# Kernel tuning notes

Hardware: AMD Instinct MI355X
Metric: run time of the kernel (lower is better)

Reference implementation:

```python
import jax, jax.numpy as jnp
import numpy as np

H = 128
EPS = 1e-5
INFERENCE_BIAS = 0.1


def setup_inputs() -> dict:
    key = jax.random.key(0)
    ks = jax.random.split(key, 10)
    n_users, n_foods, E = 100000, 50000, 1000000
    z_user = jax.random.normal(ks[0], (n_users, H), dtype=jnp.float32)
    z_food = jax.random.normal(ks[1], (n_foods, H), dtype=jnp.float32)
    row = jax.random.randint(ks[2], (E,), 0, n_users, dtype=jnp.int64)
    col = jax.random.randint(ks[3], (E,), 0, n_foods, dtype=jnp.int64)
    # lin1: Linear(2H -> H); lin2: Linear(H -> 1)
    W1 = jax.random.normal(ks[4], (H, 2 * H), dtype=jnp.float32) * (1.0 / np.sqrt(2 * H))
    b1 = jnp.zeros((H,), dtype=jnp.float32)
    gamma = jnp.ones((H,), dtype=jnp.float32)
    beta = jnp.zeros((H,), dtype=jnp.float32)
    running_mean = jax.random.normal(ks[5], (H,), dtype=jnp.float32) * 0.1
    running_var = jnp.abs(jax.random.normal(ks[6], (H,), dtype=jnp.float32)) * 0.1 + 1.0
    W2 = jax.random.normal(ks[7], (1, H), dtype=jnp.float32) * (1.0 / np.sqrt(H))
    b2 = jnp.zeros((1,), dtype=jnp.float32)
    return {"z_user": z_user, "z_food": z_food, "row": row, "col": col,
            "W1": W1, "b1": b1, "gamma": gamma, "beta": beta,
            "running_mean": running_mean, "running_var": running_var,
            "W2": W2, "b2": b2}


def reference(z_user, z_food, row, col, W1, b1, gamma, beta,
              running_mean, running_var, W2, b2):
    # gather per-edge endpoint embeddings and concat: [E, 2H]
    z = jnp.concatenate([z_user[row], z_food[col]], axis=-1)
    h = z @ W1.T + b1                                        # [E, H]
    # BatchNorm1d in eval mode: running statistics
    h = (h - running_mean) * jax.lax.rsqrt(running_var + EPS) * gamma + beta
    h = jax.nn.relu(h)                                        # dropout is identity in eval
    out = h @ W2.T + b2                                       # [E, 1]
    return jax.nn.sigmoid((out + INFERENCE_BIAS).reshape(-1)) # [E]
```

## Files before the change

### kernel.cpp

```cpp
#include <hip/hip_runtime.h>
#include <hip/hip_bf16.h>
#include <math.h>

#define H 128
#define EPS 1e-5f
#define INF_BIAS 0.1f

typedef __attribute__((ext_vector_type(8))) short bf16x8;
typedef __attribute__((ext_vector_type(4))) float f32x4;

__device__ inline unsigned short f2bf_rne(float f) {
    unsigned u = __float_as_uint(f);
    u += 0x7fffu + ((u >> 16) & 1u);
    return (unsigned short)(u >> 16);
}
__device__ inline float bf2f(unsigned short h) {
    return __uint_as_float(((unsigned)h) << 16);
}
__device__ inline unsigned pack2(float a, float b) {
    return (unsigned)f2bf_rne(a) | ((unsigned)f2bf_rne(b) << 16);
}
__device__ inline float2 unpack2(unsigned v) {
    float2 r;
    r.x = __uint_as_float(v << 16);
    r.y = __uint_as_float(v & 0xffff0000u);
    return r;
}

__global__ void prep_kernel(
    const float* __restrict__ W1, const float* __restrict__ b1,
    const float* __restrict__ gamma, const float* __restrict__ beta,
    const float* __restrict__ rm, const float* __restrict__ rv,
    unsigned short* __restrict__ Whi_u, unsigned short* __restrict__ Whi_f,
    float* __restrict__ d_user)
{
    int j = blockIdx.x;
    int k = threadIdx.x;
    float a = gamma[j] * rsqrtf(rv[j] + EPS);
    Whi_u[j * H + k] = f2bf_rne(a * W1[(size_t)j * (2 * H) + k]);
    Whi_f[j * H + k] = f2bf_rne(a * W1[(size_t)j * (2 * H) + H + k]);
    if (k == 0) d_user[j] = a * (b1[j] - rm[j]) + beta[j];
}

__global__ __launch_bounds__(256, 2) void proj_mfma(
    const float* __restrict__ z_user, const float* __restrict__ z_food,
    const unsigned short* __restrict__ Whi_u, const unsigned short* __restrict__ Whi_f,
    const float* __restrict__ d_user,
    unsigned short* __restrict__ U, unsigned short* __restrict__ F,
    int n_users, int n_foods, int GU, int GB)
{
    const bool userMode = (blockIdx.x < (unsigned)GU);
    const float* Z;
    const unsigned short* Wt;
    unsigned short* Out;
    int n, blk0, nblk;
    if (userMode) { Z = z_user; Wt = Whi_u; Out = U; n = n_users; blk0 = blockIdx.x;      nblk = GU; }
    else          { Z = z_food; Wt = Whi_f; Out = F; n = n_foods; blk0 = blockIdx.x - GU; nblk = GB - GU; }
    const int tiles = (n + 15) >> 4;

    const int wave = threadIdx.x >> 6;
    const int lane = threadIdx.x & 63;
    const int c = lane & 15;
    const int q = lane >> 4;

    bf16x8 wf[8][4];
    #pragma unroll
    for (int nt = 0; nt < 8; ++nt)
        #pragma unroll
        for (int kt = 0; kt < 4; ++kt)
            wf[nt][kt] = *(const bf16x8*)(Wt + (size_t)(nt * 16 + c) * H + kt * 32 + q * 8);

    f32x4 dvec[8];
    #pragma unroll
    for (int nt = 0; nt < 8; ++nt) {
        if (userMode) {
            float4 d = *(const float4*)(d_user + nt * 16 + q * 4);
            dvec[nt] = (f32x4){d.x, d.y, d.z, d.w};
        } else {
            dvec[nt] = (f32x4){0.f, 0.f, 0.f, 0.f};
        }
    }

    const int wid = blk0 * 4 + wave;
    const int nw  = nblk * 4;

    for (int t = wid; t < tiles; t += nw) {
        const int r = t * 16 + c;
        const float* zrow = Z + (size_t)min(r, n - 1) * H;

        f32x4 acc[8];
        #pragma unroll
        for (int nt = 0; nt < 8; ++nt) acc[nt] = dvec[nt];

        #pragma unroll
        for (int kt = 0; kt < 4; ++kt) {
            const int k0 = kt * 32 + q * 8;
            float4 za = ((const float4*)(zrow + k0))[0];
            float4 zb = ((const float4*)(zrow + k0))[1];
            bf16x8 zhi, zlo;
            {
                float v[8] = {za.x, za.y, za.z, za.w, zb.x, zb.y, zb.z, zb.w};
                #pragma unroll
                for (int i = 0; i < 8; ++i) {
                    unsigned short hi = f2bf_rne(v[i]);
                    unsigned short lo = f2bf_rne(v[i] - bf2f(hi));
                    zhi[i] = (short)hi; zlo[i] = (short)lo;
                }
            }
            #pragma unroll
            for (int nt = 0; nt < 8; ++nt) {
                acc[nt] = __builtin_amdgcn_mfma_f32_16x16x32_bf16(wf[nt][kt], zhi, acc[nt], 0, 0, 0);
                acc[nt] = __builtin_amdgcn_mfma_f32_16x16x32_bf16(wf[nt][kt], zlo, acc[nt], 0, 0, 0);
            }
        }

        if (r < n) {
            unsigned short* orow = Out + (size_t)r * H + q * 4;
            #pragma unroll
            for (int nt = 0; nt < 8; ++nt) {
                uint2 p;
                p.x = pack2(acc[nt][0], acc[nt][1]);
                p.y = pack2(acc[nt][2], acc[nt][3]);
                *(uint2*)(orow + nt * 16) = p;
            }
        }
    }
}

__global__ __launch_bounds__(256) void edge_kernel(
    const unsigned short* __restrict__ U, const unsigned short* __restrict__ F,
    const int* __restrict__ row, const int* __restrict__ col,
    const float* __restrict__ W2, const float* __restrict__ b2,
    float* __restrict__ out, int E)
{
    const int lane = threadIdx.x & 15;
    const int g       = (blockIdx.x * blockDim.x + threadIdx.x) >> 4;
    const int nGroups = (gridDim.x * blockDim.x) >> 4;

    const float4 w2a = ((const float4*)W2)[2 * lane];
    const float4 w2b = ((const float4*)W2)[2 * lane + 1];
    const float bias = b2[0] + INF_BIAS;

    for (int e = g; e < E; e += nGroups) {
        int u = row[e];
        int f = col[e];
        uint4 uv = ((const uint4*)(U + (size_t)u * H))[lane];
        uint4 fv = ((const uint4*)(F + (size_t)f * H))[lane];

        float2 u0 = unpack2(uv.x), f0 = unpack2(fv.x);
        float2 u1 = unpack2(uv.y), f1 = unpack2(fv.y);
        float2 u2 = unpack2(uv.z), f2 = unpack2(fv.z);
        float2 u3 = unpack2(uv.w), f3 = unpack2(fv.w);

        float s =
            w2a.x * fmaxf(u0.x + f0.x, 0.0f) +
            w2a.y * fmaxf(u0.y + f0.y, 0.0f) +
            w2a.z * fmaxf(u1.x + f1.x, 0.0f) +
            w2a.w * fmaxf(u1.y + f1.y, 0.0f) +
            w2b.x * fmaxf(u2.x + f2.x, 0.0f) +
            w2b.y * fmaxf(u2.y + f2.y, 0.0f) +
            w2b.z * fmaxf(u3.x + f3.x, 0.0f) +
            w2b.w * fmaxf(u3.y + f3.y, 0.0f);

        s += __shfl_xor(s, 8, 16);
        s += __shfl_xor(s, 4, 16);
        s += __shfl_xor(s, 2, 16);
        s += __shfl_xor(s, 1, 16);

        if (lane == 0) {
            float x = s + bias;
            out[e] = 1.0f / (1.0f + __expf(-x));
        }
    }
}

extern "C" void kernel_launch(void* const* d_in, const int* in_sizes, int n_in,
                              void* d_out, int out_size, void* d_ws, size_t ws_size,
                              hipStream_t stream) {
    const float* z_user = (const float*)d_in[0];
    const float* z_food = (const float*)d_in[1];
    const int*   row    = (const int*)d_in[2];
    const int*   col    = (const int*)d_in[3];
    const float* W1     = (const float*)d_in[4];
    const float* b1     = (const float*)d_in[5];
    const float* gamma  = (const float*)d_in[6];
    const float* beta   = (const float*)d_in[7];
    const float* rm     = (const float*)d_in[8];
    const float* rv     = (const float*)d_in[9];
    const float* W2     = (const float*)d_in[10];
    const float* b2     = (const float*)d_in[11];
    float* out = (float*)d_out;

    const int n_users = in_sizes[0] / H;
    const int n_foods = in_sizes[1] / H;
    const int E       = in_sizes[2];

    unsigned short* U     = (unsigned short*)d_ws;
    unsigned short* F     = U + (size_t)n_users * H;
    unsigned short* Whi_u = F + (size_t)n_foods * H;
    unsigned short* Whi_f = Whi_u + H * H;
    float*          d_usr = (float*)(Whi_f + H * H);

    prep_kernel<<<H, H, 0, stream>>>(W1, b1, gamma, beta, rm, rv,
                                     Whi_u, Whi_f, d_usr);

    const int GU = 344, GB = 516;
    proj_mfma<<<GB, 256, 0, stream>>>(z_user, z_food, Whi_u, Whi_f, d_usr,
                                      U, F, n_users, n_foods, GU, GB);

    edge_kernel<<<8192, 256, 0, stream>>>(U, F, row, col, W2, b2, out, E);
}
```

Baseline: 223.8 us.

## Stage swizzled W1 fragments in LDS to cut registers and raise occupancy

The prep kernel now writes the scaled bf16 W1 halves in MFMA-fragment order, so each projection block can copy them into shared memory with coalesced uint4 loads. Weight fragments are read from LDS per MFMA rather than held as 32 bf16x8 registers, which lowers register pressure and allows launch bounds of 4 blocks per SIMD and a grid of 1024 blocks. All four K-slices of the z row are loaded and split into hi/lo before the MFMA loop. In exchange, every tile adds LDS reads and each block pays a shared-memory fill.

```diff
diff --git a/kernel.cpp b/kernel.cpp
--- a/kernel.cpp
+++ b/kernel.cpp
@@ -31,44 +31,62 @@
     const float* __restrict__ W1, const float* __restrict__ b1,
     const float* __restrict__ gamma, const float* __restrict__ beta,
     const float* __restrict__ rm, const float* __restrict__ rv,
-    unsigned short* __restrict__ Whi_u, unsigned short* __restrict__ Whi_f,
+    unsigned short* __restrict__ Wswz_u, unsigned short* __restrict__ Wswz_f,
     float* __restrict__ d_user)
 {
-    int j = blockIdx.x;
-    int k = threadIdx.x;
-    float a = gamma[j] * rsqrtf(rv[j] + EPS);
-    Whi_u[j * H + k] = f2bf_rne(a * W1[(size_t)j * (2 * H) + k]);
-    Whi_f[j * H + k] = f2bf_rne(a * W1[(size_t)j * (2 * H) + H + k]);
-    if (k == 0) d_user[j] = a * (b1[j] - rm[j]) + beta[j];
-}
-
-__global__ __launch_bounds__(256, 2) void proj_mfma(
+    const int f  = blockIdx.x;
+    const int nt = f >> 2, kt = f & 3;
+    const int t  = threadIdx.x;
+    const int c  = t & 15, q = t >> 4;
+
+    const int j  = nt * 16 + c;
+    const float a = gamma[j] * rsqrtf(rv[j] + EPS);
+    const int k0 = kt * 32 + q * 8;
+
+    unsigned short wu[8], wf[8];
+    #pragma unroll
+    for (int i = 0; i < 8; ++i) {
+        wu[i] = f2bf_rne(a * W1[(size_t)j * (2 * H) + k0 + i]);
+        wf[i] = f2bf_rne(a * W1[(size_t)j * (2 * H) + H + k0 + i]);
+    }
+    const size_t dst = (size_t)f * 1024 / 2 + (size_t)t * 8;
+    #pragma unroll
+    for (int i = 0; i < 8; ++i) { Wswz_u[dst + i] = wu[i]; Wswz_f[dst + i] = wf[i]; }
+
+    if (kt == 0 && q == 0) d_user[j] = a * (b1[j] - rm[j]) + beta[j];
+}
+
+__global__ __launch_bounds__(256, 4) void proj_mfma(
     const float* __restrict__ z_user, const float* __restrict__ z_food,
-    const unsigned short* __restrict__ Whi_u, const unsigned short* __restrict__ Whi_f,
+    const unsigned short* __restrict__ Wswz_u, const unsigned short* __restrict__ Wswz_f,
     const float* __restrict__ d_user,
     unsigned short* __restrict__ U, unsigned short* __restrict__ F,
     int n_users, int n_foods, int GU, int GB)
 {
+    __shared__ unsigned short Wlds[32 * 64 * 8];
+
     const bool userMode = (blockIdx.x < (unsigned)GU);
     const float* Z;
-    const unsigned short* Wt;
+    const unsigned short* Wsrc;
     unsigned short* Out;
     int n, blk0, nblk;
-    if (userMode) { Z = z_user; Wt = Whi_u; Out = U; n = n_users; blk0 = blockIdx.x;      nblk = GU; }
-    else          { Z = z_food; Wt = Whi_f; Out = F; n = n_foods; blk0 = blockIdx.x - GU; nblk = GB - GU; }
+    if (userMode) { Z = z_user; Wsrc = Wswz_u; Out = U; n = n_users; blk0 = blockIdx.x;      nblk = GU; }
+    else          { Z = z_food; Wsrc = Wswz_f; Out = F; n = n_foods; blk0 = blockIdx.x - GU; nblk = GB - GU; }
     const int tiles = (n + 15) >> 4;
+
+    {
+        const uint4* src = (const uint4*)Wsrc;
+        uint4* dst = (uint4*)Wlds;
+        #pragma unroll
+        for (int i = 0; i < 8; ++i)
+            dst[i * 256 + threadIdx.x] = src[i * 256 + threadIdx.x];
+    }
+    __syncthreads();
 
     const int wave = threadIdx.x >> 6;
     const int lane = threadIdx.x & 63;
     const int c = lane & 15;
     const int q = lane >> 4;
-
-    bf16x8 wf[8][4];
-    #pragma unroll
-    for (int nt = 0; nt < 8; ++nt)
-        #pragma unroll
-        for (int kt = 0; kt < 4; ++kt)
-            wf[nt][kt] = *(const bf16x8*)(Wt + (size_t)(nt * 16 + c) * H + kt * 32 + q * 8);
 
     f32x4 dvec[8];
     #pragma unroll
@@ -88,29 +106,32 @@
         const int r = t * 16 + c;
         const float* zrow = Z + (size_t)min(r, n - 1) * H;
 
-        f32x4 acc[8];
-        #pragma unroll
-        for (int nt = 0; nt < 8; ++nt) acc[nt] = dvec[nt];
-
+        bf16x8 zhi[4], zlo[4];
         #pragma unroll
         for (int kt = 0; kt < 4; ++kt) {
             const int k0 = kt * 32 + q * 8;
             float4 za = ((const float4*)(zrow + k0))[0];
             float4 zb = ((const float4*)(zrow + k0))[1];
-            bf16x8 zhi, zlo;
-            {
-                float v[8] = {za.x, za.y, za.z, za.w, zb.x, zb.y, zb.z, zb.w};
-                #pragma unroll
-                for (int i = 0; i < 8; ++i) {
-                    unsigned short hi = f2bf_rne(v[i]);
-                    unsigned short lo = f2bf_rne(v[i] - bf2f(hi));
-                    zhi[i] = (short)hi; zlo[i] = (short)lo;
-                }
+            float v[8] = {za.x, za.y, za.z, za.w, zb.x, zb.y, zb.z, zb.w};
+            #pragma unroll
+            for (int i = 0; i < 8; ++i) {
+                unsigned short hi = f2bf_rne(v[i]);
+                unsigned short lo = f2bf_rne(v[i] - bf2f(hi));
+                zhi[kt][i] = (short)hi; zlo[kt][i] = (short)lo;
             }
+        }
+
+        f32x4 acc[8];
+        #pragma unroll
+        for (int nt = 0; nt < 8; ++nt) acc[nt] = dvec[nt];
+
+        #pragma unroll
+        for (int kt = 0; kt < 4; ++kt) {
             #pragma unroll
             for (int nt = 0; nt < 8; ++nt) {
-                acc[nt] = __builtin_amdgcn_mfma_f32_16x16x32_bf16(wf[nt][kt], zhi, acc[nt], 0, 0, 0);
-                acc[nt] = __builtin_amdgcn_mfma_f32_16x16x32_bf16(wf[nt][kt], zlo, acc[nt], 0, 0, 0);
+                bf16x8 wv = *(const bf16x8*)&Wlds[((nt * 4 + kt) * 64 + lane) * 8];
+                acc[nt] = __builtin_amdgcn_mfma_f32_16x16x32_bf16(wv, zhi[kt], acc[nt], 0, 0, 0);
+                acc[nt] = __builtin_amdgcn_mfma_f32_16x16x32_bf16(wv, zlo[kt], acc[nt], 0, 0, 0);
             }
         }
 
@@ -195,17 +216,17 @@
     const int n_foods = in_sizes[1] / H;
     const int E       = in_sizes[2];
 
-    unsigned short* U     = (unsigned short*)d_ws;
-    unsigned short* F     = U + (size_t)n_users * H;
-    unsigned short* Whi_u = F + (size_t)n_foods * H;
-    unsigned short* Whi_f = Whi_u + H * H;
-    float*          d_usr = (float*)(Whi_f + H * H);
-
-    prep_kernel<<<H, H, 0, stream>>>(W1, b1, gamma, beta, rm, rv,
-                                     Whi_u, Whi_f, d_usr);
-
-    const int GU = 344, GB = 516;
-    proj_mfma<<<GB, 256, 0, stream>>>(z_user, z_food, Whi_u, Whi_f, d_usr,
+    unsigned short* U      = (unsigned short*)d_ws;
+    unsigned short* F      = U + (size_t)n_users * H;
+    unsigned short* Wswz_u = F + (size_t)n_foods * H;
+    unsigned short* Wswz_f = Wswz_u + H * H;
+    float*          d_usr  = (float*)(Wswz_f + H * H);
+
+    prep_kernel<<<32, 64, 0, stream>>>(W1, b1, gamma, beta, rm, rv,
+                                       Wswz_u, Wswz_f, d_usr);
+
+    const int GU = 683, GB = 1024;
+    proj_mfma<<<GB, 256, 0, stream>>>(z_user, z_food, Wswz_u, Wswz_f, d_usr,
                                       U, F, n_users, n_foods, GU, GB);
 
     edge_kernel<<<8192, 256, 0, stream>>>(U, F, row, col, W2, b2, out, E);
```

After: 305.1 us. +36.3%, slower.
